# Optimization experiments

Measured on AMD Instinct MI355X. Metric: run time of the kernel, lower is better.

Reference implementation:

```python
import jax, jax.numpy as jnp
import numpy as np

N_NODES = 50000
N_EDGES = 1000000
IN_F = 128
OUT_F = 128
K = 4
NEG_SLOPE = 0.01  # torch nn.LeakyReLU() default
EPS = 1e-8


def setup_inputs() -> dict:
    key = jax.random.key(0)
    k1, k2, k3, k4, k5, k6 = jax.random.split(key, 6)
    x = jax.random.normal(k1, (N_NODES, IN_F), dtype=jnp.float32)
    e = jax.random.uniform(k2, (N_NODES, K), dtype=jnp.float32)
    stdv = 1.0 / np.sqrt(OUT_F)
    weights = jax.random.uniform(k3, (K, IN_F, OUT_F), minval=-stdv, maxval=stdv, dtype=jnp.float32)
    a = jax.random.normal(k4, (K, 2 * OUT_F, 1), dtype=jnp.float32) * 0.1
    # edge_index with no self-loops (remove_self_loops is then a no-op)
    row = jax.random.randint(k5, (N_EDGES,), 0, N_NODES)
    off = jax.random.randint(k6, (N_EDGES,), 1, N_NODES)
    col = (row + off) % N_NODES
    adj = jnp.stack([row, col]).astype(jnp.int64)
    return {"x": x, "e": e, "weights": weights, "a": a, "adj": adj}


def _canet_gat_forward(x, e, weights, a, adj):
    N = x.shape[0]
    out_f = weights.shape[-1]
    # add self loops (input has none)
    loops = jnp.arange(N, dtype=adj.dtype)
    src = jnp.concatenate([adj[0], loops])  # [Et]
    dst = jnp.concatenate([adj[1], loops])  # [Et]

    # per-head projection: [K, N, O]
    h = jnp.einsum('nd,kdo->kno', x, weights)

    # attention logits: a = [a_src; a_dst], logit_e = leakyrelu(h[src].a_src + h[dst].a_dst)
    a_src = a[:, :out_f, 0]   # [K, O]
    a_dst = a[:, out_f:, 0]   # [K, O]
    s_src = jnp.einsum('kno,ko->kn', h, a_src)  # [K, N]
    s_dst = jnp.einsum('kno,ko->kn', h, a_dst)  # [K, N]
    logits = s_src[:, src] + s_dst[:, dst]      # [K, Et]
    logits = jnp.where(logits >= 0, logits, NEG_SLOPE * logits)
    logits_max = jnp.max(logits, axis=1, keepdims=True)  # global max per head
    edge_e = jnp.exp(logits - logits_max)                # [K, Et]

    outputs = []
    for k in range(h.shape[0]):  # small fixed loop over heads (avoids [K,Et,O] blowup)
        denom = jax.ops.segment_sum(edge_e[k], src, num_segments=N) + EPS   # [N]
        msg = edge_e[k][:, None] * h[k][dst]                                # [Et, O]
        hi_k = jax.ops.segment_sum(msg, src, num_segments=N)                # [N, O]
        outputs.append(hi_k / denom[:, None])
    outputs = jnp.stack(outputs, axis=1)  # [N, K, O]

    out = jnp.sum(e[:, :, None] * outputs, axis=1)  # [N, O]
    return out + x  # residual (in_features == out_features)


def reference(x, e, weights, a, adj):
    return _canet_gat_forward(x, e, weights, a, adj)
```

## Files before the change

kernel.cpp:

```cpp
#include <hip/hip_runtime.h>
#include <hip/hip_bf16.h>
#include <cstddef>

#define NN 50000
#define NE 1000000
#define F  128
#define KH 4
#define NEG 0.01f
#define EPSF 1e-8f
#define CAP 64
#define NBIN 196
#define BINCAP 8192
#define EPB 16384
#define SUBS 4
#define NCH ((NE + EPB - 1) / EPB)
#define NB1 (NCH * SUBS)
#define NBW 256
#define NBP 2048
#define STR (NBP * 4)
#define MXSTR 32
#define TSTR 32

typedef short bf16x8 __attribute__((ext_vector_type(8)));
typedef float f32x4 __attribute__((ext_vector_type(4)));

__device__ inline ushort f2bf(float f) {
    __hip_bfloat16 b = __float2bfloat16(f);
    return *reinterpret_cast<ushort*>(&b);
}
__device__ inline unsigned int packbf(float xl, float xh) {
    return (unsigned int)f2bf(xl) | ((unsigned int)f2bf(xh) << 16);
}
__device__ inline float lk(float v) { return (v >= 0.f) ? v : NEG * v; }

__global__ __launch_bounds__(256) void bin_kernel(const int* __restrict__ adj,
                                                  int* __restrict__ binTail,
                                                  unsigned int* __restrict__ binbuf,
                                                  const float* __restrict__ W,
                                                  const float* __restrict__ a,
                                                  ushort* __restrict__ wt,
                                                  float* __restrict__ vvg) {
    int b = blockIdx.x;
    int tid = threadIdx.x;
    if (b < NB1) {
        __shared__ int hist[NBIN];
        int chunk = b >> 2, sub = b & (SUBS - 1);
        int base = chunk * EPB;
        int nloc = min(EPB, NE - base);
        for (int i = tid; i < NBIN; i += 256) hist[i] = 0;
        __syncthreads();
        for (int off0 = 0; off0 < EPB; off0 += 256 * 8) {
            int sv[8]; bool va[8];
#pragma unroll
            for (int u = 0; u < 8; u++) {
                int off = off0 + u * 256 + tid;
                va[u] = off < nloc;
                sv[u] = adj[base + (va[u] ? off : 0)];
            }
#pragma unroll
            for (int u = 0; u < 8; u++) {
                int bn = ((unsigned int)sv[u]) >> 8;
                if (va[u] && (bn & (SUBS - 1)) == sub) atomicAdd(&hist[bn], 1);
            }
        }
        __syncthreads();
        for (int i = tid; i < NBIN; i += 256) {
            if ((i & (SUBS - 1)) == sub) {
                int c = hist[i];
                hist[i] = atomicAdd(&binTail[i * TSTR], c);
            }
        }
        __syncthreads();
        for (int off0 = 0; off0 < EPB; off0 += 256 * 8) {
            int sv[8], dv[8]; bool va[8];
#pragma unroll
            for (int u = 0; u < 8; u++) {
                int off = off0 + u * 256 + tid;
                va[u] = off < nloc;
                int e = base + (va[u] ? off : 0);
                sv[u] = adj[e];
                dv[u] = adj[NE + e];
            }
#pragma unroll
            for (int u = 0; u < 8; u++) {
                unsigned int s = (unsigned int)sv[u];
                int bn = s >> 8;
                if (va[u] && (bn & (SUBS - 1)) == sub) {
                    int p = atomicAdd(&hist[bn], 1);
                    if (p < BINCAP) binbuf[(size_t)bn * BINCAP + p] = (s << 16) | (unsigned int)dv[u];
                }
            }
        }
    } else if (b < NB1 + NBW) {
        int i = (b - NB1) * 256 + tid;
        int k = i >> 14;
        int dd = (i >> 7) & 127;
        int o = i & 127;
        wt[((size_t)k * F + o) * F + dd] = f2bf(W[i]);
    } else {
        int j0 = tid * 4;
#pragma unroll
        for (int ii = 0; ii < 4; ii++) {
            int j = j0 + ii;
            int side = j >> 9;
            int k = (j >> 7) & 3;
            int dd = j & 127;
            const float4* Wr = (const float4*)(W + (size_t)k * F * F + (size_t)dd * F);
            const float4* ar = (const float4*)(a + (size_t)k * 2 * F + side * F);
            float acc = 0.f;
#pragma unroll 8
            for (int o = 0; o < F / 4; o++) {
                float4 wv = Wr[o], av = ar[o];
                acc += wv.x * av.x + wv.y * av.y + wv.z * av.z + wv.w * av.w;
            }
            vvg[j] = acc;
        }
    }
}

__global__ __launch_bounds__(256) void build_prep_kernel(const int* __restrict__ binTail,
                                                         const unsigned int* __restrict__ binbuf,
                                                         int* __restrict__ cnt,
                                                         ushort* __restrict__ bucket16,
                                                         const float* __restrict__ vvg,
                                                         const float* __restrict__ x,
                                                         unsigned int* __restrict__ xb2,
                                                         float* __restrict__ ssrc4,
                                                         float* __restrict__ sdst4,
                                                         int* __restrict__ mxsi) {
    int tid = threadIdx.x;
    __shared__ __align__(16) int shmem[1024];
    __shared__ float bmax_s[4][8];

    if (blockIdx.x < NBIN) {
        int b = blockIdx.x;
        int* lcnt = shmem;
        int* lpos = shmem + 256;
        lcnt[tid] = 0;
        lpos[tid] = 0;
        __syncthreads();
        int tail = min(binTail[b * TSTR], BINCAP);
        const unsigned int* bb = binbuf + (size_t)b * BINCAP;
        for (int i = tid; i < tail; i += 256) {
            unsigned int pk = bb[i];
            atomicAdd(&lcnt[(pk >> 16) & 255], 1);
        }
        __syncthreads();
        int n0 = b << 8;
        cnt[n0 + tid] = lcnt[tid];
        for (int i = tid; i < tail; i += 256) {
            unsigned int pk = bb[i];
            int sl = (pk >> 16) & 255;
            int p = atomicAdd(&lpos[sl], 1);
            if (p < CAP) bucket16[(size_t)(n0 + sl) * CAP + p] = (ushort)(pk & 0xffffu);
        }
        return;
    }

    float* vvf = (float*)shmem;
    ((float4*)vvf)[tid] = ((const float4*)vvg)[tid];
    __syncthreads();

    int wv = tid >> 6, lane = tid & 63;
    int gw = (blockIdx.x - NBIN) * 4 + wv;
    const float2* x2 = (const float2*)x;
    float2 vs[4], vd[4];
#pragma unroll
    for (int k = 0; k < 4; k++) {
        vs[k] = *(const float2*)&vvf[k * F + 2 * lane];
        vd[k] = *(const float2*)&vvf[(4 + k) * F + 2 * lane];
    }
    int l1 = lane & 1, l2 = lane & 2, l4 = lane & 4;
    int j = 4 * l1 + l2 + (l4 >> 2);
    float* sp = (j < 4) ? (ssrc4 + j) : (sdst4 + (j - 4));
    float mxv = 0.f;

    for (int n = gw; n < NN; n += 2 * STR) {
        int nb = n + STR;
        bool vb = nb < NN;
        float2 xa = x2[(size_t)n * 64 + lane];
        float2 xbv = vb ? x2[(size_t)nb * 64 + lane] : make_float2(0.f, 0.f);
        xb2[(size_t)n * 64 + lane] = packbf(xa.x, xa.y);
        if (vb) xb2[(size_t)nb * 64 + lane] = packbf(xbv.x, xbv.y);
        float s[8], q[8];
#pragma unroll
        for (int k = 0; k < 4; k++) {
            s[k]     = xa.x * vs[k].x + xa.y * vs[k].y;
            s[4 + k] = xa.x * vd[k].x + xa.y * vd[k].y;
            q[k]     = xbv.x * vs[k].x + xbv.y * vs[k].y;
            q[4 + k] = xbv.x * vd[k].x + xbv.y * vd[k].y;
        }
        float tA[4], tB[4];
#pragma unroll
        for (int i = 0; i < 4; i++) {
            float mA = l1 ? s[4 + i] : s[i];
            float oA = __shfl_xor(l1 ? s[i] : s[4 + i], 1);
            tA[i] = mA + oA;
            float mB = l1 ? q[4 + i] : q[i];
            float oB = __shfl_xor(l1 ? q[i] : q[4 + i], 1);
            tB[i] = mB + oB;
        }
        float uA[2], uB[2];
#pragma unroll
        for (int i = 0; i < 2; i++) {
            float mA = l2 ? tA[2 + i] : tA[i];
            float oA = __shfl_xor(l2 ? tA[i] : tA[2 + i], 2);
            uA[i] = mA + oA;
            float mB = l2 ? tB[2 + i] : tB[i];
            float oB = __shfl_xor(l2 ? tB[i] : tB[2 + i], 2);
            uB[i] = mB + oB;
        }
        float vA, vB;
        {
            float mA = l4 ? uA[1] : uA[0];
            float oA = __shfl_xor(l4 ? uA[0] : uA[1], 4);
            vA = mA + oA;
            float mB = l4 ? uB[1] : uB[0];
            float oB = __shfl_xor(l4 ? uB[0] : uB[1], 4);
            vB = mB + oB;
        }
        vA += __shfl_xor(vA, 8);  vB += __shfl_xor(vB, 8);
        vA += __shfl_xor(vA, 16); vB += __shfl_xor(vB, 16);
        vA += __shfl_xor(vA, 32); vB += __shfl_xor(vB, 32);
        if (lane < 8) {
            sp[(size_t)n * 4] = vA;
            if (vb) sp[(size_t)nb * 4] = vB;
        }
        mxv = fmaxf(mxv, fmaxf(vA, vB));
    }
    if (lane < 8) bmax_s[wv][j] = mxv;
    __syncthreads();
    if (tid < 8) {
        float m = fmaxf(fmaxf(bmax_s[0][tid], bmax_s[1][tid]),
                        fmaxf(bmax_s[2][tid], bmax_s[3][tid]));
        atomicMax(&mxsi[tid * MXSTR], __float_as_int(m));
    }
}

__global__ __launch_bounds__(256) void aggregate_kernel(const unsigned int* __restrict__ xb2,
                                                        const float* __restrict__ ssrc4,
                                                        const float* __restrict__ sdst4,
                                                        const float* __restrict__ mxs,
                                                        const int* __restrict__ cnt,
                                                        const ushort* __restrict__ bucket16,
                                                        const float* __restrict__ ew,
                                                        unsigned int* __restrict__ z2) {
    int wv = threadIdx.x >> 6, lane = threadIdx.x & 63;
    int n = blockIdx.x * 4 + wv;
    if (n >= NN) return;

    __shared__ int dsh[4][64];
    __shared__ __align__(16) float wsh[4][64][4];

    float m0 = lk(mxs[0 * MXSTR] + mxs[4 * MXSTR]);
    float m1 = lk(mxs[1 * MXSTR] + mxs[5 * MXSTR]);
    float m2 = lk(mxs[2 * MXSTR] + mxs[6 * MXSTR]);
    float m3 = lk(mxs[3 * MXSTR] + mxs[7 * MXSTR]);
    float4 ss  = *(const float4*)&ssrc4[(size_t)n * 4];
    float4 sdn = *(const float4*)&sdst4[(size_t)n * 4];
    float w0s = __expf(lk(ss.x + sdn.x) - m0);
    float w1s = __expf(lk(ss.y + sdn.y) - m1);
    float w2s = __expf(lk(ss.z + sdn.z) - m2);
    float w3s = __expf(lk(ss.w + sdn.w) - m3);

    int deg = min(cnt[n], CAP);
    float4 w = make_float4(0.f, 0.f, 0.f, 0.f);
    int d = 0;
    if (lane < deg) {
        d = (int)bucket16[(size_t)n * CAP + lane];
        float4 sd = *(const float4*)&sdst4[(size_t)d * 4];
        w.x = __expf(lk(ss.x + sd.x) - m0);
        w.y = __expf(lk(ss.y + sd.y) - m1);
        w.z = __expf(lk(ss.z + sd.z) - m2);
        w.w = __expf(lk(ss.w + sd.w) - m3);
    }
    dsh[wv][lane] = d;
    *(float4*)&wsh[wv][lane][0] = w;

    float dn0 = w.x, dn1 = w.y, dn2 = w.z, dn3 = w.w;
#pragma unroll
    for (int st = 1; st < 64; st <<= 1) {
        dn0 += __shfl_xor(dn0, st);
        dn1 += __shfl_xor(dn1, st);
        dn2 += __shfl_xor(dn2, st);
        dn3 += __shfl_xor(dn3, st);
    }

    float a0[4], a1[4];
    {
        unsigned int v = xb2[(size_t)n * 64 + lane];
        union { unsigned int u; float f; } lo, hi;
        lo.u = v << 16;
        hi.u = v & 0xffff0000u;
        a0[0] = w0s * lo.f; a1[0] = w0s * hi.f;
        a0[1] = w1s * lo.f; a1[1] = w1s * hi.f;
        a0[2] = w2s * lo.f; a1[2] = w2s * hi.f;
        a0[3] = w3s * lo.f; a1[3] = w3s * hi.f;
    }

    int degp = (deg + 15) & ~15;
    for (int i = 0; i < degp; i += 16) {
        int du[16];
#pragma unroll
        for (int u = 0; u < 16; u++)
            du[u] = __builtin_amdgcn_readfirstlane(dsh[wv][i + u]);
        unsigned int vu[16];
#pragma unroll
        for (int u = 0; u < 16; u++)
            vu[u] = xb2[(size_t)du[u] * 64 + lane];
#pragma unroll
        for (int u = 0; u < 16; u++) {
            float4 w4 = *(const float4*)&wsh[wv][i + u][0];
            union { unsigned int uu; float f; } lo, hi;
            lo.uu = vu[u] << 16;
            hi.uu = vu[u] & 0xffff0000u;
            a0[0] += w4.x * lo.f; a1[0] += w4.x * hi.f;
            a0[1] += w4.y * lo.f; a1[1] += w4.y * hi.f;
            a0[2] += w4.z * lo.f; a1[2] += w4.z * hi.f;
            a0[3] += w4.w * lo.f; a1[3] += w4.w * hi.f;
        }
    }

    float4 e4 = *(const float4*)&ew[(size_t)n * 4];
    float i0 = e4.x / (w0s + dn0 + EPSF);
    float i1 = e4.y / (w1s + dn1 + EPSF);
    float i2 = e4.z / (w2s + dn2 + EPSF);
    float i3 = e4.w / (w3s + dn3 + EPSF);
    size_t zb = (size_t)n * 256;
    z2[zb +   0 + lane] = packbf(a0[0] * i0, a1[0] * i0);
    z2[zb +  64 + lane] = packbf(a0[1] * i1, a1[1] * i1);
    z2[zb + 128 + lane] = packbf(a0[2] * i2, a1[2] * i2);
    z2[zb + 192 + lane] = packbf(a0[3] * i3, a1[3] * i3);
}

#define MT 64
__global__ __launch_bounds__(256) void gemm2_kernel(const ushort* __restrict__ z,
                                                    const ushort* __restrict__ wt,
                                                    const float* __restrict__ x,
                                                    float* __restrict__ out) {
    int row0 = blockIdx.x * MT;
    int tid = threadIdx.x;
    int wave = tid >> 6, lane = tid & 63;
    int quad = lane >> 4, l16 = lane & 15;
    __shared__ ushort ws[F][136];

    int arow = row0 + wave * 16 + l16;
    if (arow >= NN) arow = NN - 1;

    f32x4 acc[8];
#pragma unroll
    for (int i = 0; i < 8; i++) acc[i] = (f32x4){0.f, 0.f, 0.f, 0.f};

    for (int k = 0; k < KH; k++) {
        __syncthreads();
        const ushort* wk = wt + (size_t)k * F * F;
        for (int i = tid; i < F * 16; i += 256) {
            int r = i >> 4, c = (i & 15) * 8;
            *(uint4*)&ws[r][c] = *(const uint4*)&wk[r * F + c];
        }
        __syncthreads();
#pragma unroll
        for (int kt = 0; kt < 4; kt++) {
            int kb = kt * 32 + quad * 8;
            bf16x8 af = *(const bf16x8*)&z[(size_t)arow * 512 + k * F + kb];
#pragma unroll
            for (int ni = 0; ni < 8; ni++) {
                bf16x8 bf = *(const bf16x8*)&ws[ni * 16 + l16][kb];
                acc[ni] = __builtin_amdgcn_mfma_f32_16x16x32_bf16(af, bf, acc[ni], 0, 0, 0);
            }
        }
    }
#pragma unroll
    for (int r = 0; r < 4; r++) {
        int n = row0 + wave * 16 + quad * 4 + r;
        if (n < NN) {
#pragma unroll
            for (int ni = 0; ni < 8; ni++) {
                int o = ni * 16 + l16;
                out[(size_t)n * F + o] = x[(size_t)n * F + o] + acc[ni][r];
            }
        }
    }
}

extern "C" void kernel_launch(void* const* d_in, const int* in_sizes, int n_in,
                              void* d_out, int out_size, void* d_ws, size_t ws_size,
                              hipStream_t stream) {
    const float* x = (const float*)d_in[0];
    const float* e = (const float*)d_in[1];
    const float* W = (const float*)d_in[2];
    const float* a = (const float*)d_in[3];
    const int*   adj = (const int*)d_in[4];
    float* out = (float*)d_out;

    char* ws = (char*)d_ws;
    auto take = [&](size_t bytes) {
        char* p = ws;
        ws += (bytes + 255) & ~(size_t)255;
        return p;
    };
    ushort* z      = (ushort*)take((size_t)NN * KH * F * sizeof(ushort));
    unsigned int* xb2 = (unsigned int*)take((size_t)NN * F * sizeof(ushort));
    ushort* wt     = (ushort*)take((size_t)KH * F * F * sizeof(ushort));
    float* ssrc4   = (float*)take((size_t)NN * 4 * sizeof(float));
    float* sdst4   = (float*)take((size_t)NN * 4 * sizeof(float));
    int*   cnt     = (int*)take((size_t)NBIN * 256 * sizeof(int));
    ushort* bucket16 = (ushort*)take((size_t)NBIN * 256 * CAP * sizeof(ushort));
    unsigned int* binbuf = (unsigned int*)take((size_t)NBIN * BINCAP * sizeof(unsigned int));
    int*   binTail = (int*)take((size_t)NBIN * TSTR * sizeof(int));
    float* mxs     = (float*)take((size_t)8 * MXSTR * sizeof(float));
    float* vvg     = (float*)take((size_t)8 * F * sizeof(float));

    hipMemsetAsync(binTail, 0, (size_t)NBIN * TSTR * sizeof(int), stream);
    hipMemsetAsync(mxs, 0, (size_t)8 * MXSTR * sizeof(float), stream);
    bin_kernel<<<NB1 + NBW + 1, 256, 0, stream>>>(adj, binTail, binbuf, W, a, wt, vvg);
    build_prep_kernel<<<NBIN + NBP, 256, 0, stream>>>(binTail, binbuf, cnt, bucket16,
                                                      vvg, x, xb2, ssrc4, sdst4, (int*)mxs);
    aggregate_kernel<<<(NN + 3) / 4, 256, 0, stream>>>(xb2, ssrc4, sdst4, mxs, cnt,
                                                       bucket16, e, (unsigned int*)z);
    gemm2_kernel<<<(NN + MT - 1) / MT, 256, 0, stream>>>(z, wt, x, out);
}
```

Before: 239.1 us.

## Regroup pipeline stages and process multiple nodes per wave in aggregation

The pipeline is reorganised into four kernels. The small vv projection now runs in its own tiny kernel. The edge binning is merged with the x-to-bf16 conversion and the score prep into one launch, so the bandwidth-bound prep can overlap with the atomic-heavy binning. Bucket building becomes a separate kernel, and the aggregation kernel now loops over 4 nodes per wave with a gather batch of 8 instead of 16. This adds one launch and may lower memory-level parallelism per wave in the gather loop.

```diff
diff --git a/kernel.cpp b/kernel.cpp
--- a/kernel.cpp
+++ b/kernel.cpp
@@ -20,6 +20,7 @@
 #define STR (NBP * 4)
 #define MXSTR 32
 #define TSTR 32
+#define NPB 16
 
 typedef short bf16x8 __attribute__((ext_vector_type(8)));
 typedef float f32x4 __attribute__((ext_vector_type(4)));
@@ -33,17 +34,46 @@
 }
 __device__ inline float lk(float v) { return (v >= 0.f) ? v : NEG * v; }
 
-__global__ __launch_bounds__(256) void bin_kernel(const int* __restrict__ adj,
-                                                  int* __restrict__ binTail,
-                                                  unsigned int* __restrict__ binbuf,
-                                                  const float* __restrict__ W,
-                                                  const float* __restrict__ a,
-                                                  ushort* __restrict__ wt,
-                                                  float* __restrict__ vvg) {
+__global__ __launch_bounds__(256) void vv_kernel(const float* __restrict__ W,
+                                                 const float* __restrict__ a,
+                                                 float* __restrict__ vvg) {
+    int j0 = threadIdx.x * 4;
+#pragma unroll
+    for (int ii = 0; ii < 4; ii++) {
+        int j = j0 + ii;
+        int side = j >> 9;
+        int k = (j >> 7) & 3;
+        int dd = j & 127;
+        const float4* Wr = (const float4*)(W + (size_t)k * F * F + (size_t)dd * F);
+        const float4* ar = (const float4*)(a + (size_t)k * 2 * F + side * F);
+        float acc = 0.f;
+#pragma unroll 8
+        for (int o = 0; o < F / 4; o++) {
+            float4 wv = Wr[o], av = ar[o];
+            acc += wv.x * av.x + wv.y * av.y + wv.z * av.z + wv.w * av.w;
+        }
+        vvg[j] = acc;
+    }
+}
+
+__global__ __launch_bounds__(256) void bin_prep_kernel(const int* __restrict__ adj,
+                                                       int* __restrict__ binTail,
+                                                       unsigned int* __restrict__ binbuf,
+                                                       const float* __restrict__ W,
+                                                       ushort* __restrict__ wt,
+                                                       const float* __restrict__ vvg,
+                                                       const float* __restrict__ x,
+                                                       unsigned int* __restrict__ xb2,
+                                                       float* __restrict__ ssrc4,
+                                                       float* __restrict__ sdst4,
+                                                       int* __restrict__ mxsi) {
     int b = blockIdx.x;
     int tid = threadIdx.x;
+    __shared__ __align__(16) int shmem[1024];
+    __shared__ float bmax_s[4][8];
+
     if (b < NB1) {
-        __shared__ int hist[NBIN];
+        int* hist = shmem;
         int chunk = b >> 2, sub = b & (SUBS - 1);
         int base = chunk * EPB;
         int nloc = min(EPB, NE - base);
@@ -91,69 +121,14 @@
                 }
             }
         }
-    } else if (b < NB1 + NBW) {
-        int i = (b - NB1) * 256 + tid;
+        return;
+    }
+    if (b >= NB1 + NBP) {
+        int i = (b - NB1 - NBP) * 256 + tid;
         int k = i >> 14;
         int dd = (i >> 7) & 127;
         int o = i & 127;
         wt[((size_t)k * F + o) * F + dd] = f2bf(W[i]);
-    } else {
-        int j0 = tid * 4;
-#pragma unroll
-        for (int ii = 0; ii < 4; ii++) {
-            int j = j0 + ii;
-            int side = j >> 9;
-            int k = (j >> 7) & 3;
-            int dd = j & 127;
-            const float4* Wr = (const float4*)(W + (size_t)k * F * F + (size_t)dd * F);
-            const float4* ar = (const float4*)(a + (size_t)k * 2 * F + side * F);
-            float acc = 0.f;
-#pragma unroll 8
-            for (int o = 0; o < F / 4; o++) {
-                float4 wv = Wr[o], av = ar[o];
-                acc += wv.x * av.x + wv.y * av.y + wv.z * av.z + wv.w * av.w;
-            }
-            vvg[j] = acc;
-        }
-    }
-}
-
-__global__ __launch_bounds__(256) void build_prep_kernel(const int* __restrict__ binTail,
-                                                         const unsigned int* __restrict__ binbuf,
-                                                         int* __restrict__ cnt,
-                                                         ushort* __restrict__ bucket16,
-                                                         const float* __restrict__ vvg,
-                                                         const float* __restrict__ x,
-                                                         unsigned int* __restrict__ xb2,
-                                                         float* __restrict__ ssrc4,
-                                                         float* __restrict__ sdst4,
-                                                         int* __restrict__ mxsi) {
-    int tid = threadIdx.x;
-    __shared__ __align__(16) int shmem[1024];
-    __shared__ float bmax_s[4][8];
-
-    if (blockIdx.x < NBIN) {
-        int b = blockIdx.x;
-        int* lcnt = shmem;
-        int* lpos = shmem + 256;
-        lcnt[tid] = 0;
-        lpos[tid] = 0;
-        __syncthreads();
-        int tail = min(binTail[b * TSTR], BINCAP);
-        const unsigned int* bb = binbuf + (size_t)b * BINCAP;
-        for (int i = tid; i < tail; i += 256) {
-            unsigned int pk = bb[i];
-            atomicAdd(&lcnt[(pk >> 16) & 255], 1);
-        }
-        __syncthreads();
-        int n0 = b << 8;
-        cnt[n0 + tid] = lcnt[tid];
-        for (int i = tid; i < tail; i += 256) {
-            unsigned int pk = bb[i];
-            int sl = (pk >> 16) & 255;
-            int p = atomicAdd(&lpos[sl], 1);
-            if (p < CAP) bucket16[(size_t)(n0 + sl) * CAP + p] = (ushort)(pk & 0xffffu);
-        }
         return;
     }
 
@@ -162,7 +137,7 @@
     __syncthreads();
 
     int wv = tid >> 6, lane = tid & 63;
-    int gw = (blockIdx.x - NBIN) * 4 + wv;
+    int gw = (b - NB1) * 4 + wv;
     const float2* x2 = (const float2*)x;
     float2 vs[4], vd[4];
 #pragma unroll
@@ -234,6 +209,34 @@
         float m = fmaxf(fmaxf(bmax_s[0][tid], bmax_s[1][tid]),
                         fmaxf(bmax_s[2][tid], bmax_s[3][tid]));
         atomicMax(&mxsi[tid * MXSTR], __float_as_int(m));
+    }
+}
+
+__global__ __launch_bounds__(256) void build_kernel(const int* __restrict__ binTail,
+                                                    const unsigned int* __restrict__ binbuf,
+                                                    int* __restrict__ cnt,
+                                                    ushort* __restrict__ bucket16) {
+    int tid = threadIdx.x;
+    __shared__ int lcnt[256];
+    __shared__ int lpos[256];
+    int b = blockIdx.x;
+    lcnt[tid] = 0;
+    lpos[tid] = 0;
+    __syncthreads();
+    int tail = min(binTail[b * TSTR], BINCAP);
+    const unsigned int* bb = binbuf + (size_t)b * BINCAP;
+    for (int i = tid; i < tail; i += 256) {
+        unsigned int pk = bb[i];
+        atomicAdd(&lcnt[(pk >> 16) & 255], 1);
+    }
+    __syncthreads();
+    int n0 = b << 8;
+    cnt[n0 + tid] = lcnt[tid];
+    for (int i = tid; i < tail; i += 256) {
+        unsigned int pk = bb[i];
+        int sl = (pk >> 16) & 255;
+        int p = atomicAdd(&lpos[sl], 1);
+        if (p < CAP) bucket16[(size_t)(n0 + sl) * CAP + p] = (ushort)(pk & 0xffffu);
     }
 }
 
@@ -246,9 +249,6 @@
                                                         const float* __restrict__ ew,
                                                         unsigned int* __restrict__ z2) {
     int wv = threadIdx.x >> 6, lane = threadIdx.x & 63;
-    int n = blockIdx.x * 4 + wv;
-    if (n >= NN) return;
-
     __shared__ int dsh[4][64];
     __shared__ __align__(16) float wsh[4][64][4];
 
@@ -256,81 +256,89 @@
     float m1 = lk(mxs[1 * MXSTR] + mxs[5 * MXSTR]);
     float m2 = lk(mxs[2 * MXSTR] + mxs[6 * MXSTR]);
     float m3 = lk(mxs[3 * MXSTR] + mxs[7 * MXSTR]);
-    float4 ss  = *(const float4*)&ssrc4[(size_t)n * 4];
-    float4 sdn = *(const float4*)&sdst4[(size_t)n * 4];
-    float w0s = __expf(lk(ss.x + sdn.x) - m0);
-    float w1s = __expf(lk(ss.y + sdn.y) - m1);
-    float w2s = __expf(lk(ss.z + sdn.z) - m2);
-    float w3s = __expf(lk(ss.w + sdn.w) - m3);
-
-    int deg = min(cnt[n], CAP);
-    float4 w = make_float4(0.f, 0.f, 0.f, 0.f);
-    int d = 0;
-    if (lane < deg) {
-        d = (int)bucket16[(size_t)n * CAP + lane];
-        float4 sd = *(const float4*)&sdst4[(size_t)d * 4];
-        w.x = __expf(lk(ss.x + sd.x) - m0);
-        w.y = __expf(lk(ss.y + sd.y) - m1);
-        w.z = __expf(lk(ss.z + sd.z) - m2);
-        w.w = __expf(lk(ss.w + sd.w) - m3);
-    }
-    dsh[wv][lane] = d;
-    *(float4*)&wsh[wv][lane][0] = w;
-
-    float dn0 = w.x, dn1 = w.y, dn2 = w.z, dn3 = w.w;
-#pragma unroll
-    for (int st = 1; st < 64; st <<= 1) {
-        dn0 += __shfl_xor(dn0, st);
-        dn1 += __shfl_xor(dn1, st);
-        dn2 += __shfl_xor(dn2, st);
-        dn3 += __shfl_xor(dn3, st);
-    }
-
-    float a0[4], a1[4];
-    {
-        unsigned int v = xb2[(size_t)n * 64 + lane];
-        union { unsigned int u; float f; } lo, hi;
-        lo.u = v << 16;
-        hi.u = v & 0xffff0000u;
-        a0[0] = w0s * lo.f; a1[0] = w0s * hi.f;
-        a0[1] = w1s * lo.f; a1[1] = w1s * hi.f;
-        a0[2] = w2s * lo.f; a1[2] = w2s * hi.f;
-        a0[3] = w3s * lo.f; a1[3] = w3s * hi.f;
-    }
-
-    int degp = (deg + 15) & ~15;
-    for (int i = 0; i < degp; i += 16) {
-        int du[16];
-#pragma unroll
-        for (int u = 0; u < 16; u++)
-            du[u] = __builtin_amdgcn_readfirstlane(dsh[wv][i + u]);
-        unsigned int vu[16];
-#pragma unroll
-        for (int u = 0; u < 16; u++)
-            vu[u] = xb2[(size_t)du[u] * 64 + lane];
-#pragma unroll
-        for (int u = 0; u < 16; u++) {
-            float4 w4 = *(const float4*)&wsh[wv][i + u][0];
-            union { unsigned int uu; float f; } lo, hi;
-            lo.uu = vu[u] << 16;
-            hi.uu = vu[u] & 0xffff0000u;
-            a0[0] += w4.x * lo.f; a1[0] += w4.x * hi.f;
-            a0[1] += w4.y * lo.f; a1[1] += w4.y * hi.f;
-            a0[2] += w4.z * lo.f; a1[2] += w4.z * hi.f;
-            a0[3] += w4.w * lo.f; a1[3] += w4.w * hi.f;
-        }
-    }
-
-    float4 e4 = *(const float4*)&ew[(size_t)n * 4];
-    float i0 = e4.x / (w0s + dn0 + EPSF);
-    float i1 = e4.y / (w1s + dn1 + EPSF);
-    float i2 = e4.z / (w2s + dn2 + EPSF);
-    float i3 = e4.w / (w3s + dn3 + EPSF);
-    size_t zb = (size_t)n * 256;
-    z2[zb +   0 + lane] = packbf(a0[0] * i0, a1[0] * i0);
-    z2[zb +  64 + lane] = packbf(a0[1] * i1, a1[1] * i1);
-    z2[zb + 128 + lane] = packbf(a0[2] * i2, a1[2] * i2);
-    z2[zb + 192 + lane] = packbf(a0[3] * i3, a1[3] * i3);
+
+    int n0 = blockIdx.x * NPB + wv * (NPB / 4);
+#pragma unroll 1
+    for (int g = 0; g < NPB / 4; ++g) {
+        int n = n0 + g;
+        if (n >= NN) break;
+
+        float4 ss  = *(const float4*)&ssrc4[(size_t)n * 4];
+        float4 sdn = *(const float4*)&sdst4[(size_t)n * 4];
+        float w0s = __expf(lk(ss.x + sdn.x) - m0);
+        float w1s = __expf(lk(ss.y + sdn.y) - m1);
+        float w2s = __expf(lk(ss.z + sdn.z) - m2);
+        float w3s = __expf(lk(ss.w + sdn.w) - m3);
+
+        int deg = min(cnt[n], CAP);
+        float4 w = make_float4(0.f, 0.f, 0.f, 0.f);
+        int d = 0;
+        if (lane < deg) {
+            d = (int)bucket16[(size_t)n * CAP + lane];
+            float4 sd = *(const float4*)&sdst4[(size_t)d * 4];
+            w.x = __expf(lk(ss.x + sd.x) - m0);
+            w.y = __expf(lk(ss.y + sd.y) - m1);
+            w.z = __expf(lk(ss.z + sd.z) - m2);
+            w.w = __expf(lk(ss.w + sd.w) - m3);
+        }
+        dsh[wv][lane] = d;
+        *(float4*)&wsh[wv][lane][0] = w;
+
+        float dn0 = w.x, dn1 = w.y, dn2 = w.z, dn3 = w.w;
+#pragma unroll
+        for (int st = 1; st < 64; st <<= 1) {
+            dn0 += __shfl_xor(dn0, st);
+            dn1 += __shfl_xor(dn1, st);
+            dn2 += __shfl_xor(dn2, st);
+            dn3 += __shfl_xor(dn3, st);
+        }
+
+        float a0[4], a1[4];
+        {
+            unsigned int v = xb2[(size_t)n * 64 + lane];
+            union { unsigned int u; float f; } lo, hi;
+            lo.u = v << 16;
+            hi.u = v & 0xffff0000u;
+            a0[0] = w0s * lo.f; a1[0] = w0s * hi.f;
+            a0[1] = w1s * lo.f; a1[1] = w1s * hi.f;
+            a0[2] = w2s * lo.f; a1[2] = w2s * hi.f;
+            a0[3] = w3s * lo.f; a1[3] = w3s * hi.f;
+        }
+
+        int degp = (deg + 7) & ~7;
+        for (int i = 0; i < degp; i += 8) {
+            int du[8];
+#pragma unroll
+            for (int u = 0; u < 8; u++)
+                du[u] = __builtin_amdgcn_readfirstlane(dsh[wv][i + u]);
+            unsigned int vu[8];
+#pragma unroll
+            for (int u = 0; u < 8; u++)
+                vu[u] = xb2[(size_t)du[u] * 64 + lane];
+#pragma unroll
+            for (int u = 0; u < 8; u++) {
+                float4 w4 = *(const float4*)&wsh[wv][i + u][0];
+                union { unsigned int uu; float f; } lo, hi;
+                lo.uu = vu[u] << 16;
+                hi.uu = vu[u] & 0xffff0000u;
+                a0[0] += w4.x * lo.f; a1[0] += w4.x * hi.f;
+                a0[1] += w4.y * lo.f; a1[1] += w4.y * hi.f;
+                a0[2] += w4.z * lo.f; a1[2] += w4.z * hi.f;
+                a0[3] += w4.w * lo.f; a1[3] += w4.w * hi.f;
+            }
+        }
+
+        float4 e4 = *(const float4*)&ew[(size_t)n * 4];
+        float i0 = e4.x / (w0s + dn0 + EPSF);
+        float i1 = e4.y / (w1s + dn1 + EPSF);
+        float i2 = e4.z / (w2s + dn2 + EPSF);
+        float i3 = e4.w / (w3s + dn3 + EPSF);
+        size_t zb = (size_t)n * 256;
+        z2[zb +   0 + lane] = packbf(a0[0] * i0, a1[0] * i0);
+        z2[zb +  64 + lane] = packbf(a0[1] * i1, a1[1] * i1);
+        z2[zb + 128 + lane] = packbf(a0[2] * i2, a1[2] * i2);
+        z2[zb + 192 + lane] = packbf(a0[3] * i3, a1[3] * i3);
+    }
 }
 
 #define MT 64
@@ -413,10 +421,11 @@
 
     hipMemsetAsync(binTail, 0, (size_t)NBIN * TSTR * sizeof(int), stream);
     hipMemsetAsync(mxs, 0, (size_t)8 * MXSTR * sizeof(float), stream);
-    bin_kernel<<<NB1 + NBW + 1, 256, 0, stream>>>(adj, binTail, binbuf, W, a, wt, vvg);
-    build_prep_kernel<<<NBIN + NBP, 256, 0, stream>>>(binTail, binbuf, cnt, bucket16,
-                                                      vvg, x, xb2, ssrc4, sdst4, (int*)mxs);
-    aggregate_kernel<<<(NN + 3) / 4, 256, 0, stream>>>(xb2, ssrc4, sdst4, mxs, cnt,
-                                                       bucket16, e, (unsigned int*)z);
+    vv_kernel<<<1, 256, 0, stream>>>(W, a, vvg);
+    bin_prep_kernel<<<NB1 + NBP + NBW, 256, 0, stream>>>(adj, binTail, binbuf, W, wt,
+                                                         vvg, x, xb2, ssrc4, sdst4, (int*)mxs);
+    build_kernel<<<NBIN, 256, 0, stream>>>(binTail, binbuf, cnt, bucket16);
+    aggregate_kernel<<<(NN + NPB - 1) / NPB, 256, 0, stream>>>(xb2, ssrc4, sdst4, mxs, cnt,
+                                                               bucket16, e, (unsigned int*)z);
     gemm2_kernel<<<(NN + MT - 1) / MT, 256, 0, stream>>>(z, wt, x, out);
 }
```

Result: no change. 240.0 us (+0.4%).
